# Kernel tuning notes

Measured on AMD Instinct MI355X. Metric: run time of the kernel, lower is better.

## Reference

```python
import jax, jax.numpy as jnp
import numpy as np

# hyperparams (match CombinedPeakLoss defaults)
ALPHA, BETA, GAMMA, DELTA, EPSILON = 1.0, 2.0, 1.0, 0.5, 0.5
PEAK_WINDOW = 2
DAYTIME_WEIGHT = 2.0
TEMPERATURE = 0.1
HOURS = 24
NEG = -1e9


def setup_inputs() -> dict:
    key = jax.random.key(0)
    k1, k2 = jax.random.split(key)
    B, S = 16384, 720  # 30 days of hourly data
    y_pred = jax.random.uniform(k1, (B, S), dtype=jnp.float32)
    y_true = jax.random.uniform(k2, (B, S), dtype=jnp.float32)
    return {"y_pred": y_pred, "y_true": y_true}


def _soft_peaks(y_bdh, day_mask, hours):
    # y_bdh: [B,D,H]; day_mask: [1,D,H] bool; hours: [H]
    masked = jnp.where(day_mask, y_bdh, NEG)
    attn = jax.nn.softmax(masked / TEMPERATURE, axis=-1)  # [B,D,H]
    peak_val = (attn * y_bdh).sum(-1)                      # [B,D]
    peak_time = (attn * hours).sum(-1)                     # [B,D]
    return peak_val, peak_time


def reference(y_pred, y_true):
    B, S = y_true.shape
    D = S // HOURS
    dt = y_true.dtype

    # default is_daytime: tiled hour-of-day, daytime = 6..20 inclusive
    t = jnp.tile(jnp.arange(HOURS), D)[:S]                 # [S]
    is_day = ((t >= 6) & (t <= 20))                        # [S] bool
    day_mask = is_day.reshape(1, D, HOURS)                 # [1,D,H]
    hours = jnp.arange(HOURS, dtype=dt)                    # [H]

    yt = y_true.reshape(B, D, HOURS)
    yp = y_pred.reshape(B, D, HOURS)

    # L_overall
    L_overall = jnp.mean((y_pred - y_true) ** 2)

    # soft peak extraction for both true and pred
    t_pv, t_pt = _soft_peaks(yt, day_mask, hours)
    p_pv, p_pt = _soft_peaks(yp, day_mask, hours)
    L_peak_value = jnp.mean((p_pv - t_pv) ** 2)
    L_peak_time = jnp.mean((p_pt - t_pt) ** 2)

    # peak shape loss: hard argmax on daytime-masked truth, windowed normalized MSE
    masked_true = jnp.where(day_mask, yt, NEG)
    peak_idx = jnp.argmax(masked_true, axis=-1)            # [B,D]
    ws = jnp.maximum(0, peak_idx - PEAK_WINDOW)            # [B,D]
    we = jnp.minimum(HOURS, peak_idx + PEAK_WINDOW + 1)    # [B,D]
    h = jnp.arange(HOURS)
    wmask = (h[None, None, :] >= ws[..., None]) & (h[None, None, :] < we[..., None])  # [B,D,H]
    tmax = jnp.max(jnp.where(wmask, yt, NEG), axis=-1)     # [B,D]
    pmax = jnp.max(jnp.where(wmask, yp, NEG), axis=-1)     # [B,D]
    valid = tmax > 1e-6
    tmax_safe = jnp.where(valid, tmax, 1.0)
    diff = yp / (pmax[..., None] + 1e-6) - yt / tmax_safe[..., None]
    wlen = (we - ws).astype(dt)
    mse_win = jnp.sum(jnp.where(wmask, diff ** 2, 0.0), axis=-1) / wlen  # [B,D]
    L_peak_shape = jnp.sum(jnp.where(valid, mse_win, 0.0)) / (jnp.sum(valid) + 1e-6)

    # daytime-weighted extra MSE
    dw = jnp.where(is_day, DAYTIME_WEIGHT, 1.0).astype(dt)  # [S]
    weighted_mse = jnp.mean((y_pred - y_true) ** 2 * dw)
    L_daytime = weighted_mse - L_overall

    total = (ALPHA * L_overall + BETA * L_peak_value + GAMMA * L_peak_time
             + DELTA * L_peak_shape + EPSILON * L_daytime)
    return total
```

## Files before the change

### kernel.cpp

```cpp
#include <hip/hip_runtime.h>
#include <hip/hip_fp16.h>

#define HOURS 24
#define RPB 256
#define PSTR 25


__global__ __launch_bounds__(256, 6) void peakloss_main(
    const float* __restrict__ ypred, const float* __restrict__ ytrue,
    float* __restrict__ partials, int nrows, int nblocks) {
  __shared__ __half2 ltp[RPB * PSTR];

  const int tid = threadIdx.x;
  const int tile0 = blockIdx.x * RPB;
  const int rows = min(RPB, nrows - tile0);

  if (rows == RPB) {
    const float4* t4 = (const float4*)(ytrue + (size_t)tile0 * HOURS);
    const float4* p4 = (const float4*)(ypred + (size_t)tile0 * HOURS);
#pragma unroll
    for (int j = 0; j < 6; ++j) {
      int f4 = tid + j * 256;
      float4 a = t4[f4];
      float4 b = p4[f4];
      int pa0 = f4 * 4 + f4 / 6;
      ltp[pa0 + 0] = __floats2half2_rn(a.x, b.x);
      ltp[pa0 + 1] = __floats2half2_rn(a.y, b.y);
      ltp[pa0 + 2] = __floats2half2_rn(a.z, b.z);
      ltp[pa0 + 3] = __floats2half2_rn(a.w, b.w);
    }
  } else {
    for (int d = tid; d < rows * HOURS; d += 256) {
      int pa = d + d / HOURS;
      ltp[pa] = __floats2half2_rn(ytrue[(size_t)tile0 * HOURS + d],
                                  ypred[(size_t)tile0 * HOURS + d]);
    }
  }
  __syncthreads();

  float s_sq = 0.f, s_day = 0.f, s_pv = 0.f, s_pt = 0.f, s_shape = 0.f, s_valid = 0.f;

  if (tid < rows) {
    const __half2* row = ltp + tid * PSTR;

    float mt = -1e30f, mp = -1e30f;
    int idx = 6;
#pragma unroll
    for (int h = 0; h < HOURS; ++h) {
      __half2 v = row[h];
      float th = __low2float(v), ph = __high2float(v);
      float d = ph - th;
      float dd = d * d;
      s_sq += dd;
      if (h >= 6 && h <= 20) {
        s_day += dd;
        if (th > mt) { mt = th; idx = h; }
        mp = fmaxf(mp, ph);
      }
    }

    int ws = idx - 2;
    float den_t = 0.f, nv_t = 0.f, nt_t = 0.f;
    float den_p = 0.f, nv_p = 0.f, nt_p = 0.f;
    float tmax = -1e30f, pmax = -1e30f;
#pragma unroll
    for (int h = 4; h <= 22; ++h) {
      __half2 v = row[h];
      float th = __low2float(v), ph = __high2float(v);
      if (h >= 6 && h <= 20) {
        float et = __expf((th - mt) * 10.f);
        den_t += et; nv_t += et * th; nt_t += et * (float)h;
        float ep = __expf((ph - mp) * 10.f);
        den_p += ep; nv_p += ep * ph; nt_p += ep * (float)h;
      }
      bool in = (h >= ws) & (h < ws + 5);
      if (in) { tmax = fmaxf(tmax, th); pmax = fmaxf(pmax, ph); }
    }
    float r_t = __builtin_amdgcn_rcpf(den_t);
    float r_p = __builtin_amdgcn_rcpf(den_p);
    float dv  = nv_p * r_p - nv_t * r_t;
    float dtm = nt_p * r_p - nt_t * r_t;
    s_pv += dv * dv;
    s_pt += dtm * dtm;

    bool valid = tmax > 1e-6f;
    float tms = valid ? tmax : 1.0f;
    float r_tms  = __builtin_amdgcn_rcpf(tms);
    float r_pden = __builtin_amdgcn_rcpf(pmax + 1e-6f);
    float a = 0.f;
#pragma unroll
    for (int h = 4; h <= 22; ++h) {
      __half2 v = row[h];
      float th = __low2float(v), ph = __high2float(v);
      bool in = (h >= ws) & (h < ws + 5);
      float d = ph * r_pden - th * r_tms;
      a += in ? d * d : 0.f;
    }
    if (valid) { s_shape += a * 0.2f; s_valid += 1.0f; }
  }

  float v[6] = {s_sq, s_day, s_pv, s_pt, s_shape, s_valid};
#pragma unroll
  for (int j = 0; j < 6; ++j) {
#pragma unroll
    for (int off = 32; off >= 1; off >>= 1) v[j] += __shfl_down(v[j], off, 64);
  }
  __shared__ float red[6][4];
  int lane = threadIdx.x & 63, wave = threadIdx.x >> 6;
  __syncthreads();
  if (lane == 0) {
#pragma unroll
    for (int j = 0; j < 6; ++j) red[j][wave] = v[j];
  }
  __syncthreads();
  if (threadIdx.x < 6) {
    int j = threadIdx.x;
    partials[(size_t)j * nblocks + blockIdx.x] =
        red[j][0] + red[j][1] + red[j][2] + red[j][3];
  }
}

__global__ __launch_bounds__(256) void peakloss_reduce(
    const float* __restrict__ partials, float* __restrict__ out,
    int nblocks, double inv_BS, double inv_BD) {
  double s[6] = {0, 0, 0, 0, 0, 0};
  for (int i = threadIdx.x; i < nblocks; i += 256) {
#pragma unroll
    for (int j = 0; j < 6; ++j) s[j] += (double)partials[(size_t)j * nblocks + i];
  }
#pragma unroll
  for (int j = 0; j < 6; ++j) {
#pragma unroll
    for (int off = 32; off >= 1; off >>= 1) s[j] += __shfl_down(s[j], off, 64);
  }
  __shared__ double red[6][4];
  int lane = threadIdx.x & 63, wave = threadIdx.x >> 6;
  if (lane == 0) {
#pragma unroll
    for (int j = 0; j < 6; ++j) red[j][wave] = s[j];
  }
  __syncthreads();
  if (threadIdx.x == 0) {
    double a[6];
#pragma unroll
    for (int j = 0; j < 6; ++j)
      a[j] = red[j][0] + red[j][1] + red[j][2] + red[j][3];
    double L_overall = a[0] * inv_BS;
    double L_day     = a[1] * inv_BS;
    double L_pv      = a[2] * inv_BD;
    double L_pt      = a[3] * inv_BD;
    double L_shape   = a[4] / (a[5] + 1e-6);
    out[0] = (float)(L_overall + 2.0 * L_pv + L_pt + 0.5 * L_shape + 0.5 * L_day);
  }
}

extern "C" void kernel_launch(void* const* d_in, const int* in_sizes, int n_in,
                              void* d_out, int out_size, void* d_ws, size_t ws_size,
                              hipStream_t stream) {
  const float* ypred = (const float*)d_in[0];
  const float* ytrue = (const float*)d_in[1];
  float* out = (float*)d_out;
  float* partials = (float*)d_ws;

  long long N = in_sizes[0];
  int nrows = (int)(N / HOURS);
  int grid = (nrows + RPB - 1) / RPB;

  peakloss_main<<<grid, 256, 0, stream>>>(ypred, ytrue, partials, nrows, grid);

  double inv_BS = 1.0 / (double)N;
  double inv_BD = 1.0 / (double)nrows;
  peakloss_reduce<<<1, 256, 0, stream>>>(partials, out, grid, inv_BS, inv_BD);
}
```

Measured before the change: 28.01 us.

## Compute MSE sums in load loop and expand shape loss algebraically

Moves the squared-error and daytime-weighted sums into the global load phase, using the full-precision float values before the half conversion, and removes them from the per-row loop. The windowed normalized MSE is rewritten as an expansion of sums of t^2, p^2 and t*p collected in the existing window pass, which removes the third pass over the row. This trades per-row LDS reads and ALU work for extra accumulators, and the expanded form can lose precision through cancellation.

After: 28.68 us. 2.4% more time.

```diff
diff --git a/kernel.cpp b/kernel.cpp
--- a/kernel.cpp
+++ b/kernel.cpp
@@ -15,6 +15,8 @@
   const int tile0 = blockIdx.x * RPB;
   const int rows = min(RPB, nrows - tile0);
 
+  float s_sq = 0.f, s_day = 0.f, s_pv = 0.f, s_pt = 0.f, s_shape = 0.f, s_valid = 0.f;
+
   if (rows == RPB) {
     const float4* t4 = (const float4*)(ytrue + (size_t)tile0 * HOURS);
     const float4* p4 = (const float4*)(ypred + (size_t)tile0 * HOURS);
@@ -28,17 +30,28 @@
       ltp[pa0 + 1] = __floats2half2_rn(a.y, b.y);
       ltp[pa0 + 2] = __floats2half2_rn(a.z, b.z);
       ltp[pa0 + 3] = __floats2half2_rn(a.w, b.w);
+      int h0 = 4 * (f4 % 6);
+      float dx = b.x - a.x, dy = b.y - a.y, dz = b.z - a.z, dw = b.w - a.w;
+      float qx = dx * dx, qy = dy * dy, qz = dz * dz, qw = dw * dw;
+      s_sq += qx + qy + qz + qw;
+      s_day += ((h0 + 0 >= 6) & (h0 + 0 <= 20)) ? qx : 0.f;
+      s_day += ((h0 + 1 >= 6) & (h0 + 1 <= 20)) ? qy : 0.f;
+      s_day += ((h0 + 2 >= 6) & (h0 + 2 <= 20)) ? qz : 0.f;
+      s_day += ((h0 + 3 >= 6) & (h0 + 3 <= 20)) ? qw : 0.f;
     }
   } else {
     for (int d = tid; d < rows * HOURS; d += 256) {
+      float tv = ytrue[(size_t)tile0 * HOURS + d];
+      float pv = ypred[(size_t)tile0 * HOURS + d];
       int pa = d + d / HOURS;
-      ltp[pa] = __floats2half2_rn(ytrue[(size_t)tile0 * HOURS + d],
-                                  ypred[(size_t)tile0 * HOURS + d]);
+      ltp[pa] = __floats2half2_rn(tv, pv);
+      float dd = (pv - tv) * (pv - tv);
+      int h = d % HOURS;
+      s_sq += dd;
+      s_day += ((h >= 6) & (h <= 20)) ? dd : 0.f;
     }
   }
   __syncthreads();
-
-  float s_sq = 0.f, s_day = 0.f, s_pv = 0.f, s_pt = 0.f, s_shape = 0.f, s_valid = 0.f;
 
   if (tid < rows) {
     const __half2* row = ltp + tid * PSTR;
@@ -46,23 +59,18 @@
     float mt = -1e30f, mp = -1e30f;
     int idx = 6;
 #pragma unroll
-    for (int h = 0; h < HOURS; ++h) {
+    for (int h = 6; h <= 20; ++h) {
       __half2 v = row[h];
       float th = __low2float(v), ph = __high2float(v);
-      float d = ph - th;
-      float dd = d * d;
-      s_sq += dd;
-      if (h >= 6 && h <= 20) {
-        s_day += dd;
-        if (th > mt) { mt = th; idx = h; }
-        mp = fmaxf(mp, ph);
-      }
+      if (th > mt) { mt = th; idx = h; }
+      mp = fmaxf(mp, ph);
     }
 
     int ws = idx - 2;
     float den_t = 0.f, nv_t = 0.f, nt_t = 0.f;
     float den_p = 0.f, nv_p = 0.f, nt_p = 0.f;
     float tmax = -1e30f, pmax = -1e30f;
+    float St2 = 0.f, Sp2 = 0.f, Stp = 0.f;
 #pragma unroll
     for (int h = 4; h <= 22; ++h) {
       __half2 v = row[h];
@@ -74,7 +82,10 @@
         den_p += ep; nv_p += ep * ph; nt_p += ep * (float)h;
       }
       bool in = (h >= ws) & (h < ws + 5);
-      if (in) { tmax = fmaxf(tmax, th); pmax = fmaxf(pmax, ph); }
+      if (in) {
+        tmax = fmaxf(tmax, th); pmax = fmaxf(pmax, ph);
+        St2 += th * th; Sp2 += ph * ph; Stp += th * ph;
+      }
     }
     float r_t = __builtin_amdgcn_rcpf(den_t);
     float r_p = __builtin_amdgcn_rcpf(den_p);
@@ -85,17 +96,9 @@
 
     bool valid = tmax > 1e-6f;
     float tms = valid ? tmax : 1.0f;
-    float r_tms  = __builtin_amdgcn_rcpf(tms);
-    float r_pden = __builtin_amdgcn_rcpf(pmax + 1e-6f);
-    float a = 0.f;
-#pragma unroll
-    for (int h = 4; h <= 22; ++h) {
-      __half2 v = row[h];
-      float th = __low2float(v), ph = __high2float(v);
-      bool in = (h >= ws) & (h < ws + 5);
-      float d = ph * r_pden - th * r_tms;
-      a += in ? d * d : 0.f;
-    }
+    float rt = __builtin_amdgcn_rcpf(tms);
+    float rp = __builtin_amdgcn_rcpf(pmax + 1e-6f);
+    float a = rp * rp * Sp2 + rt * rt * St2 - 2.f * rp * rt * Stp;
     if (valid) { s_shape += a * 0.2f; s_valid += 1.0f; }
   }
 
```
